# Performance work log

Measured on AMD Instinct MI355X. Metric: run time of the kernel, lower is better.

## Reference

```python
import jax, jax.numpy as jnp
import numpy as np

N = 100000   # num nodes
E = 600000   # num edges (avg degree 6)
H = 8        # num_heads
D = 16       # out_dim
T = 20000    # minibatch target nodes


def setup_inputs() -> dict:
    key = jax.random.key(0)
    k1, k2, k3, k4 = jax.random.split(key, 4)
    node = jax.random.normal(k1, (N, H, D), dtype=jnp.float32)
    eft = jax.random.normal(k2, (E, H, D), dtype=jnp.float32)
    dst = jax.random.randint(k3, (E,), 0, N, dtype=jnp.int32)
    target_idx = jax.random.randint(k4, (T,), 0, N, dtype=jnp.int32)
    return {"node": node, "eft": eft, "dst": dst, "target_idx": target_idx}


def reference(node, eft, dst, target_idx):
    # e_mul_v: edge feature * gathered destination node feature, [E,H,D]
    m = eft * node[dst]
    sim = m.sum(axis=-1)                              # [E,H]
    # NOTE: forward applies F.softmax over dim=-1 (the HEADS axis), per source.
    a = jax.nn.softmax(sim, axis=-1)[..., None]        # [E,H,1]
    # message passing: scatter-sum of eft * a into destination nodes
    nft = jax.ops.segment_sum(eft * a, dst, num_segments=node.shape[0])  # [N,H,D]
    v = nft.reshape(-1, H, D)
    x = v[target_idx] + 1e-15                           # [T,H,D]
    # F.normalize(x, 2): L2-normalize over dim=1 (heads), eps=1e-12
    norm = jnp.sqrt(jnp.sum(x * x, axis=1, keepdims=True))
    out = x / jnp.maximum(norm, 1e-12)
    return out, a
```

## Files before the change

kernel.cpp:

```cpp
#include <hip/hip_runtime.h>
#include <hip/hip_bf16.h>
#include <math.h>

#define HH 8
#define DD 16
#define HD 128

__global__ void __launch_bounds__(256) mark_zero_kernel(
    const int* __restrict__ tidx,
    unsigned char* __restrict__ mark,
    float* __restrict__ nft,
    int T)
{
    int wave = (int)((blockIdx.x * blockDim.x + threadIdx.x) >> 6);
    int lane = threadIdx.x & 63;
    if (wave >= T) return;
    int n = tidx[wave];
    if (lane == 0) mark[n] = 1;
    float2* p = (float2*)(nft + (size_t)n * HD);
    p[lane] = make_float2(0.0f, 0.0f);
}

__global__ void __launch_bounds__(256) edge_kernel(
    const float* __restrict__ node,
    const float* __restrict__ eft,
    const int*   __restrict__ dst,
    const unsigned char* __restrict__ mark,
    float*       __restrict__ nft,
    float*       __restrict__ a_out,
    int E)
{
    int w    = (int)((blockIdx.x * blockDim.x + threadIdx.x) >> 6);
    int lane = threadIdx.x & 63;
    int e    = 2 * w + (lane >> 5);
    if (e >= E) return;
    const int dn = dst[e];

    float4 ev = ((const float4*)eft)[(size_t)e * 32 + (lane & 31)];
    float4 nv = ((const float4*)node)[(size_t)dn * 32 + (lane & 31)];

    float p = ev.x * nv.x + ev.y * nv.y + ev.z * nv.z + ev.w * nv.w;
    p += __shfl_xor(p, 1);
    p += __shfl_xor(p, 2);

    float ex = __expf(p);
    float s = ex;
    s += __shfl_xor(s, 4);
    s += __shfl_xor(s, 8);
    s += __shfl_xor(s, 16);
    float a = __fdividef(ex, s);

    if ((lane & 3) == 0)
        a_out[(size_t)e * HH + ((lane >> 2) & 7)] = a;

    if (mark[dn]) {
        float* dp = nft + (size_t)dn * HD + (lane & 31) * 4;
        atomicAdd(dp,     ev.x * a);
        atomicAdd(dp + 1, ev.y * a);
        atomicAdd(dp + 2, ev.z * a);
        atomicAdd(dp + 3, ev.w * a);
    }
}

__global__ void __launch_bounds__(256) target_kernel(
    const float* __restrict__ nft,
    const int*   __restrict__ target_idx,
    float*       __restrict__ out,
    int T)
{
    int w    = (int)((blockIdx.x * blockDim.x + threadIdx.x) >> 6);
    int lane = threadIdx.x & 63;
    if (w >= T) return;
    int n = target_idx[w];
    float2 x = ((const float2*)(nft + (size_t)n * HD))[lane];
    x.x += 1e-15f;
    x.y += 1e-15f;
    float sx = x.x * x.x;
    float sy = x.y * x.y;
    sx += __shfl_xor(sx, 8);  sy += __shfl_xor(sy, 8);
    sx += __shfl_xor(sx, 16); sy += __shfl_xor(sy, 16);
    sx += __shfl_xor(sx, 32); sy += __shfl_xor(sy, 32);
    float2 o;
    o.x = x.x / fmaxf(sqrtf(sx), 1e-12f);
    o.y = x.y / fmaxf(sqrtf(sy), 1e-12f);
    ((float2*)(out + (size_t)w * HD))[lane] = o;
}

extern "C" void kernel_launch(void* const* d_in, const int* in_sizes, int n_in,
                              void* d_out, int out_size, void* d_ws, size_t ws_size,
                              hipStream_t stream)
{
    const float* node = (const float*)d_in[0];
    const float* eft  = (const float*)d_in[1];
    const int*   dst  = (const int*)d_in[2];
    const int*   tidx = (const int*)d_in[3];

    const int N = in_sizes[0] / HD;
    const int E = in_sizes[2];
    const int T = in_sizes[3];

    float* out   = (float*)d_out;
    float* a_out = out + (size_t)T * HD;
    float* nft   = (float*)d_ws;

    unsigned char* mark = (unsigned char*)d_out;

    hipMemsetAsync(mark, 0, (size_t)N, stream);

    {
        int blocks = (T + 3) / 4;
        mark_zero_kernel<<<blocks, 256, 0, stream>>>(tidx, mark, nft, T);
    }

    {
        int waves = (E + 1) / 2;
        int blocks = (waves + 3) / 4;
        edge_kernel<<<blocks, 256, 0, stream>>>(node, eft, dst, mark, nft, a_out, E);
    }

    {
        int blocks = (T + 3) / 4;
        target_kernel<<<blocks, 256, 0, stream>>>(nft, tidx, out, T);
    }
}
```

Measured before the change: 556.5 us.

## Process four edges per wave in grid-stride loop with scalar dst loads

Measured after the change: 479.5 us. 1.16x faster.

```diff
diff --git a/kernel.cpp b/kernel.cpp
--- a/kernel.cpp
+++ b/kernel.cpp
@@ -30,35 +30,102 @@
     float*       __restrict__ a_out,
     int E)
 {
-    int w    = (int)((blockIdx.x * blockDim.x + threadIdx.x) >> 6);
-    int lane = threadIdx.x & 63;
-    int e    = 2 * w + (lane >> 5);
-    if (e >= E) return;
-    const int dn = dst[e];
+    const int lane   = threadIdx.x & 63;
+    const int wid    = (int)((blockIdx.x * blockDim.x + threadIdx.x) >> 6);
+    const int nwaves = (int)((gridDim.x * blockDim.x) >> 6);
 
-    float4 ev = ((const float4*)eft)[(size_t)e * 32 + (lane & 31)];
-    float4 nv = ((const float4*)node)[(size_t)dn * 32 + (lane & 31)];
+    for (int base = wid * 4; base < E; base += nwaves * 4) {
+        if (base + 3 < E) {
+            int4 d4 = *(const int4*)(dst + base);
+            int dn0 = __builtin_amdgcn_readfirstlane(d4.x);
+            int dn1 = __builtin_amdgcn_readfirstlane(d4.y);
+            int dn2 = __builtin_amdgcn_readfirstlane(d4.z);
+            int dn3 = __builtin_amdgcn_readfirstlane(d4.w);
 
-    float p = ev.x * nv.x + ev.y * nv.y + ev.z * nv.z + ev.w * nv.w;
-    p += __shfl_xor(p, 1);
-    p += __shfl_xor(p, 2);
+            const float2* ep = (const float2*)(eft + (size_t)base * HD);
+            float2 ev0 = ep[lane];
+            float2 ev1 = ep[64 + lane];
+            float2 ev2 = ep[128 + lane];
+            float2 ev3 = ep[192 + lane];
+            float2 nv0 = ((const float2*)(node + (size_t)dn0 * HD))[lane];
+            float2 nv1 = ((const float2*)(node + (size_t)dn1 * HD))[lane];
+            float2 nv2 = ((const float2*)(node + (size_t)dn2 * HD))[lane];
+            float2 nv3 = ((const float2*)(node + (size_t)dn3 * HD))[lane];
 
-    float ex = __expf(p);
-    float s = ex;
-    s += __shfl_xor(s, 4);
-    s += __shfl_xor(s, 8);
-    s += __shfl_xor(s, 16);
-    float a = __fdividef(ex, s);
+            float p0 = ev0.x * nv0.x + ev0.y * nv0.y;
+            float p1 = ev1.x * nv1.x + ev1.y * nv1.y;
+            float p2 = ev2.x * nv2.x + ev2.y * nv2.y;
+            float p3 = ev3.x * nv3.x + ev3.y * nv3.y;
+            p0 += __shfl_xor(p0, 1); p1 += __shfl_xor(p1, 1);
+            p2 += __shfl_xor(p2, 1); p3 += __shfl_xor(p3, 1);
+            p0 += __shfl_xor(p0, 2); p1 += __shfl_xor(p1, 2);
+            p2 += __shfl_xor(p2, 2); p3 += __shfl_xor(p3, 2);
+            p0 += __shfl_xor(p0, 4); p1 += __shfl_xor(p1, 4);
+            p2 += __shfl_xor(p2, 4); p3 += __shfl_xor(p3, 4);
 
-    if ((lane & 3) == 0)
-        a_out[(size_t)e * HH + ((lane >> 2) & 7)] = a;
+            float x0 = __expf(p0), x1 = __expf(p1);
+            float x2 = __expf(p2), x3 = __expf(p3);
+            float s0 = x0, s1 = x1, s2 = x2, s3 = x3;
+            s0 += __shfl_xor(s0, 8);  s1 += __shfl_xor(s1, 8);
+            s2 += __shfl_xor(s2, 8);  s3 += __shfl_xor(s3, 8);
+            s0 += __shfl_xor(s0, 16); s1 += __shfl_xor(s1, 16);
+            s2 += __shfl_xor(s2, 16); s3 += __shfl_xor(s3, 16);
+            s0 += __shfl_xor(s0, 32); s1 += __shfl_xor(s1, 32);
+            s2 += __shfl_xor(s2, 32); s3 += __shfl_xor(s3, 32);
+            float a0 = __fdividef(x0, s0);
+            float a1 = __fdividef(x1, s1);
+            float a2 = __fdividef(x2, s2);
+            float a3 = __fdividef(x3, s3);
 
-    if (mark[dn]) {
-        float* dp = nft + (size_t)dn * HD + (lane & 31) * 4;
-        atomicAdd(dp,     ev.x * a);
-        atomicAdd(dp + 1, ev.y * a);
-        atomicAdd(dp + 2, ev.z * a);
-        atomicAdd(dp + 3, ev.w * a);
+            if ((lane & 7) == 0) {
+                int h = lane >> 3;
+                float* ap = a_out + (size_t)base * HH + h;
+                ap[0]  = a0;
+                ap[8]  = a1;
+                ap[16] = a2;
+                ap[24] = a3;
+            }
+
+            if (mark[dn0]) {
+                float* dp = nft + (size_t)dn0 * HD + lane * 2;
+                atomicAdd(dp, ev0.x * a0); atomicAdd(dp + 1, ev0.y * a0);
+            }
+            if (mark[dn1]) {
+                float* dp = nft + (size_t)dn1 * HD + lane * 2;
+                atomicAdd(dp, ev1.x * a1); atomicAdd(dp + 1, ev1.y * a1);
+            }
+            if (mark[dn2]) {
+                float* dp = nft + (size_t)dn2 * HD + lane * 2;
+                atomicAdd(dp, ev2.x * a2); atomicAdd(dp + 1, ev2.y * a2);
+            }
+            if (mark[dn3]) {
+                float* dp = nft + (size_t)dn3 * HD + lane * 2;
+                atomicAdd(dp, ev3.x * a3); atomicAdd(dp + 1, ev3.y * a3);
+            }
+        } else {
+            for (int e = base; e < E; e++) {
+                int dn = __builtin_amdgcn_readfirstlane(dst[e]);
+                float2 ev = ((const float2*)(eft + (size_t)e * HD))[lane];
+                float2 nv = ((const float2*)(node + (size_t)dn * HD))[lane];
+                float p = ev.x * nv.x + ev.y * nv.y;
+                p += __shfl_xor(p, 1);
+                p += __shfl_xor(p, 2);
+                p += __shfl_xor(p, 4);
+                float ex = __expf(p);
+                float s = ex;
+                s += __shfl_xor(s, 8);
+                s += __shfl_xor(s, 16);
+                s += __shfl_xor(s, 32);
+                float a = __fdividef(ex, s);
+                if ((lane & 7) == 0)
+                    a_out[(size_t)e * HH + (lane >> 3)] = a;
+                if (mark[dn]) {
+                    float* dp = nft + (size_t)dn * HD + lane * 2;
+                    atomicAdd(dp, ev.x * a);
+                    atomicAdd(dp + 1, ev.y * a);
+                }
+            }
+        }
     }
 }
 
@@ -113,8 +180,7 @@
     }
 
     {
-        int waves = (E + 1) / 2;
-        int blocks = (waves + 3) / 4;
+        int blocks = 2048;
         edge_kernel<<<blocks, 256, 0, stream>>>(node, eft, dst, mark, nft, a_out, E);
     }
 
```
